# Kernel tuning notes

Measured on AMD Instinct MI355X. Metric: run time of the kernel, lower is better.

The kernel has to match this reference:

```python
import jax, jax.numpy as jnp
import numpy as np

B, CIN, H, W = 16, 32, 256, 256
COUT, KH, KW = 32, 3, 3
NUM_EXPERTS = 8
PAD = ((1, 1), (1, 1))  # static 'same' padding for 3x3, stride 1, dilation 1


def setup_inputs() -> dict:
    key = jax.random.key(0)
    k_x, k_r, k_w, k_b = jax.random.split(key, 4)
    x = jax.random.normal(k_x, (B, CIN, H, W), dtype=jnp.float32)
    # routing weights are typically sigmoid/softmax outputs in [0,1]
    routing_weights = jax.nn.softmax(jax.random.normal(k_r, (B, NUM_EXPERTS), dtype=jnp.float32), axis=-1)
    num_params = COUT * CIN * KH * KW  # groups=1 -> in_channels//groups = CIN
    expert_weight = jax.random.normal(k_w, (NUM_EXPERTS, num_params), dtype=jnp.float32) * 0.05
    expert_bias = jax.random.normal(k_b, (NUM_EXPERTS, COUT), dtype=jnp.float32) * 0.05
    return {"x": x, "routing_weights": routing_weights,
            "expert_weight": expert_weight, "expert_bias": expert_bias}


def reference(x, routing_weights, expert_weight, expert_bias):
    b = x.shape[0]
    # Per-sample kernels: [B, num_params] -> [B, COUT, CIN, KH, KW]
    w = jnp.matmul(routing_weights, expert_weight).reshape(b, COUT, CIN, KH, KW)
    bias = jnp.matmul(routing_weights, expert_bias)  # [B, COUT]

    def conv_one(xi, wi):
        # xi: [CIN, H, W], wi: [COUT, CIN, KH, KW]
        return jax.lax.conv_general_dilated(
            xi[None], wi, window_strides=(1, 1), padding=PAD,
            dimension_numbers=("NCHW", "OIHW", "NCHW"))[0]

    out = jax.vmap(conv_one)(x, w)  # [B, COUT, H, W]
    out = out + bias[:, :, None, None]
    return out
```

## Files before the change

kernel.cpp:

```cpp
#include <hip/hip_runtime.h>

#define B_   16
#define CIN  32
#define COUT 32
#define HH   256
#define WW   256
#define NE   8
#define NTAP 9
#define KTOT (NTAP * CIN)

#define TH 8
#define TW 64
#define LROWS (TH + 2)
#define LCOLS (TW + 2)
#define PXS   40
#define NI    ((TW + 8) / 4)

typedef __attribute__((ext_vector_type(8))) short  short8;
typedef __attribute__((ext_vector_type(4))) float  floatx4;

__device__ __forceinline__ unsigned short f2bf(float f) {
    unsigned int u = __float_as_uint(f);
    u += 0x7FFFu + ((u >> 16) & 1u);
    return (unsigned short)(u >> 16);
}

__global__ __launch_bounds__(256) void prep_weights(
    const float* __restrict__ routing,
    const float* __restrict__ ew,
    const float* __restrict__ eb,
    unsigned short* __restrict__ ws_w,
    float* __restrict__ ws_b)
{
    const int b = blockIdx.x;
    const int t = threadIdx.x;
    float r[NE];
#pragma unroll
    for (int e = 0; e < NE; ++e) r[e] = routing[b * NE + e];

    for (int idx = t; idx < COUT * KTOT; idx += 256) {
        const int co  = idx / KTOT;
        const int k   = idx - co * KTOT;
        const int tap = k >> 5;
        const int ci  = k & 31;
        float acc = 0.f;
#pragma unroll
        for (int e = 0; e < NE; ++e)
            acc += r[e] * ew[e * (COUT * CIN * 9) + co * (CIN * 9) + ci * 9 + tap];
        ws_w[(b * COUT + co) * KTOT + k] = f2bf(acc);
    }
    if (t < COUT) {
        float acc = 0.f;
#pragma unroll
        for (int e = 0; e < NE; ++e) acc += r[e] * eb[e * COUT + t];
        ws_b[b * COUT + t] = acc;
    }
}

__global__ __launch_bounds__(256, 3) void condconv_mfma(
    const float* __restrict__ x,
    const unsigned short* __restrict__ wsw,
    const float* __restrict__ wsb,
    float* __restrict__ out)
{
    __shared__ __align__(16) unsigned short s_x[LROWS * LCOLS * PXS];

    const int b    = blockIdx.z;
    const int x0   = blockIdx.x * TW;
    const int y0   = blockIdx.y * TH;
    const int t    = threadIdx.x;
    const int lane = t & 63;
    const int wv   = t >> 6;
    const int ln   = lane & 15;
    const int quad = lane >> 4;

    for (int task = t; task < LROWS * NI * 4; task += 256) {
        const int cg  = task & 3;
        const int ri  = task >> 2;
        const int i   = ri % NI;
        const int row = ri / NI;
        const int gy  = y0 + row - 1;
        const int gx  = x0 + 4 * i - 4;
        floatx4 v[8];
        if (gy >= 0 && gy < HH && gx >= 0 && gx < WW) {
            const float* src = x + (((size_t)b * CIN + cg * 8) * HH + gy) * WW + gx;
#pragma unroll
            for (int u = 0; u < 8; ++u)
                v[u] = *(const floatx4*)(src + (size_t)u * HH * WW);
        } else {
#pragma unroll
            for (int u = 0; u < 8; ++u) v[u] = (floatx4){0.f, 0.f, 0.f, 0.f};
        }
#pragma unroll
        for (int j = 0; j < 4; ++j) {
            const int lcol = 4 * i + j - 3;
            if (lcol >= 0 && lcol < LCOLS) {
                short8 pk;
#pragma unroll
                for (int u = 0; u < 8; ++u) pk[u] = (short)f2bf(v[u][j]);
                *(short8*)&s_x[(row * LCOLS + lcol) * PXS + cg * 8] = pk;
            }
        }
    }

    const unsigned short* wb = wsw + (size_t)b * COUT * KTOT;
    short8 afc0 = *(const short8*)(wb + ln * KTOT + quad * 8);
    short8 afc1 = *(const short8*)(wb + (16 + ln) * KTOT + quad * 8);

    floatx4 acc[8][2];
#pragma unroll
    for (int tt = 0; tt < 8; ++tt)
#pragma unroll
        for (int h = 0; h < 2; ++h)
            acc[tt][h] = (floatx4){0.f, 0.f, 0.f, 0.f};

    int base[8];
#pragma unroll
    for (int tt = 0; tt < 8; ++tt)
        base[tt] = ((2 * wv + (tt >> 2)) * LCOLS + (tt & 3) * 16 + ln) * PXS + quad * 8;

    __syncthreads();

#pragma unroll 1
    for (int tap = 0; tap < NTAP; ++tap) {
        const int tn = (tap < NTAP - 1) ? tap + 1 : NTAP - 1;
        const short8 afn0 = *(const short8*)(wb + ln * KTOT + tn * 32 + quad * 8);
        const short8 afn1 = *(const short8*)(wb + (16 + ln) * KTOT + tn * 32 + quad * 8);
        const int dy  = tap / 3;
        const int dx  = tap - dy * 3;
        const int off = (dy * LCOLS + dx) * PXS;
#pragma unroll
        for (int tt = 0; tt < 8; ++tt) {
            const short8 bfr = *(const short8*)&s_x[base[tt] + off];
            acc[tt][0] = __builtin_amdgcn_mfma_f32_16x16x32_bf16(afc0, bfr, acc[tt][0], 0, 0, 0);
            acc[tt][1] = __builtin_amdgcn_mfma_f32_16x16x32_bf16(afc1, bfr, acc[tt][1], 0, 0, 0);
        }
        afc0 = afn0;
        afc1 = afn1;
    }

    float bias_v[2][4];
#pragma unroll
    for (int h = 0; h < 2; ++h)
#pragma unroll
        for (int rg = 0; rg < 4; ++rg)
            bias_v[h][rg] = wsb[b * COUT + h * 16 + quad * 4 + rg];

#pragma unroll
    for (int tt = 0; tt < 8; ++tt) {
        const int r  = 2 * wv + (tt >> 2);
        const int q  = tt & 3;
        const int gy = y0 + r;
        const int gx = x0 + q * 16 + ln;
#pragma unroll
        for (int h = 0; h < 2; ++h)
#pragma unroll
            for (int rg = 0; rg < 4; ++rg) {
                const int co = h * 16 + quad * 4 + rg;
                out[(((size_t)b * COUT + co) * HH + gy) * WW + gx] = acc[tt][h][rg] + bias_v[h][rg];
            }
    }
}

extern "C" void kernel_launch(void* const* d_in, const int* in_sizes, int n_in,
                              void* d_out, int out_size, void* d_ws, size_t ws_size,
                              hipStream_t stream) {
    const float* x       = (const float*)d_in[0];
    const float* routing = (const float*)d_in[1];
    const float* ew      = (const float*)d_in[2];
    const float* eb      = (const float*)d_in[3];
    float* out = (float*)d_out;

    unsigned short* ws_w = (unsigned short*)d_ws;
    float* ws_b = (float*)((char*)d_ws + (size_t)B_ * COUT * KTOT * 2);

    prep_weights<<<dim3(B_), dim3(256), 0, stream>>>(routing, ew, eb, ws_w, ws_b);

    dim3 grid(WW / TW, HH / TH, B_);
    condconv_mfma<<<grid, dim3(256), 0, stream>>>(x, ws_w, ws_b, out);
}
```

Before: 287.2 us.

## Swap MFMA operands for vectorized stores and halve tile width

Swaps the MFMA A/B operands so pixels are the row dimension and output channels the column dimension. Each lane then holds four consecutive x positions for one output channel and writes them as a single 16-byte store instead of scattered scalar stores. The tile width is halved to 32 and the occupancy hint raised to 5 blocks per CU, which gives more, smaller blocks. The cost is more halo overhead per block, since the input tile is still loaded with a 2-column halo on each side for only 32 columns.

```diff
diff --git a/kernel.cpp b/kernel.cpp
--- a/kernel.cpp
+++ b/kernel.cpp
@@ -10,7 +10,7 @@
 #define KTOT (NTAP * CIN)
 
 #define TH 8
-#define TW 64
+#define TW 32
 #define LROWS (TH + 2)
 #define LCOLS (TW + 2)
 #define PXS   40
@@ -57,7 +57,7 @@
     }
 }
 
-__global__ __launch_bounds__(256, 3) void condconv_mfma(
+__global__ __launch_bounds__(256, 5) void condconv_mfma(
     const float* __restrict__ x,
     const unsigned short* __restrict__ wsw,
     const float* __restrict__ wsb,
@@ -104,61 +104,57 @@
     }
 
     const unsigned short* wb = wsw + (size_t)b * COUT * KTOT;
-    short8 afc0 = *(const short8*)(wb + ln * KTOT + quad * 8);
-    short8 afc1 = *(const short8*)(wb + (16 + ln) * KTOT + quad * 8);
+    short8 wfc0 = *(const short8*)(wb + ln * KTOT + quad * 8);
+    short8 wfc1 = *(const short8*)(wb + (16 + ln) * KTOT + quad * 8);
 
-    floatx4 acc[8][2];
+    floatx4 acc[4][2];
 #pragma unroll
-    for (int tt = 0; tt < 8; ++tt)
+    for (int tt = 0; tt < 4; ++tt)
 #pragma unroll
         for (int h = 0; h < 2; ++h)
             acc[tt][h] = (floatx4){0.f, 0.f, 0.f, 0.f};
 
-    int base[8];
+    int base[4];
 #pragma unroll
-    for (int tt = 0; tt < 8; ++tt)
-        base[tt] = ((2 * wv + (tt >> 2)) * LCOLS + (tt & 3) * 16 + ln) * PXS + quad * 8;
+    for (int tt = 0; tt < 4; ++tt)
+        base[tt] = ((2 * wv + (tt >> 1)) * LCOLS + (tt & 1) * 16 + ln) * PXS + quad * 8;
 
     __syncthreads();
 
 #pragma unroll 1
     for (int tap = 0; tap < NTAP; ++tap) {
         const int tn = (tap < NTAP - 1) ? tap + 1 : NTAP - 1;
-        const short8 afn0 = *(const short8*)(wb + ln * KTOT + tn * 32 + quad * 8);
-        const short8 afn1 = *(const short8*)(wb + (16 + ln) * KTOT + tn * 32 + quad * 8);
+        const short8 wfn0 = *(const short8*)(wb + ln * KTOT + tn * 32 + quad * 8);
+        const short8 wfn1 = *(const short8*)(wb + (16 + ln) * KTOT + tn * 32 + quad * 8);
         const int dy  = tap / 3;
         const int dx  = tap - dy * 3;
         const int off = (dy * LCOLS + dx) * PXS;
 #pragma unroll
-        for (int tt = 0; tt < 8; ++tt) {
-            const short8 bfr = *(const short8*)&s_x[base[tt] + off];
-            acc[tt][0] = __builtin_amdgcn_mfma_f32_16x16x32_bf16(afc0, bfr, acc[tt][0], 0, 0, 0);
-            acc[tt][1] = __builtin_amdgcn_mfma_f32_16x16x32_bf16(afc1, bfr, acc[tt][1], 0, 0, 0);
+        for (int tt = 0; tt < 4; ++tt) {
+            const short8 pfr = *(const short8*)&s_x[base[tt] + off];
+            acc[tt][0] = __builtin_amdgcn_mfma_f32_16x16x32_bf16(pfr, wfc0, acc[tt][0], 0, 0, 0);
+            acc[tt][1] = __builtin_amdgcn_mfma_f32_16x16x32_bf16(pfr, wfc1, acc[tt][1], 0, 0, 0);
         }
-        afc0 = afn0;
-        afc1 = afn1;
+        wfc0 = wfn0;
+        wfc1 = wfn1;
     }
 
-    float bias_v[2][4];
-#pragma unroll
-    for (int h = 0; h < 2; ++h)
-#pragma unroll
-        for (int rg = 0; rg < 4; ++rg)
-            bias_v[h][rg] = wsb[b * COUT + h * 16 + quad * 4 + rg];
+    float bias_v[2];
+    bias_v[0] = wsb[b * COUT + ln];
+    bias_v[1] = wsb[b * COUT + 16 + ln];
 
 #pragma unroll
-    for (int tt = 0; tt < 8; ++tt) {
-        const int r  = 2 * wv + (tt >> 2);
-        const int q  = tt & 3;
-        const int gy = y0 + r;
-        const int gx = x0 + q * 16 + ln;
+    for (int tt = 0; tt < 4; ++tt) {
+        const int gy = y0 + 2 * wv + (tt >> 1);
+        const int gx = x0 + (tt & 1) * 16 + quad * 4;
 #pragma unroll
-        for (int h = 0; h < 2; ++h)
+        for (int h = 0; h < 2; ++h) {
+            floatx4 vo = acc[tt][h];
 #pragma unroll
-            for (int rg = 0; rg < 4; ++rg) {
-                const int co = h * 16 + quad * 4 + rg;
-                out[(((size_t)b * COUT + co) * HH + gy) * WW + gx] = acc[tt][h][rg] + bias_v[h][rg];
-            }
+            for (int e = 0; e < 4; ++e) vo[e] += bias_v[h];
+            const int co = h * 16 + ln;
+            *(floatx4*)(out + (((size_t)b * COUT + co) * HH + gy) * WW + gx) = vo;
+        }
     }
 }
 
```

New measurement: 289.0 us. About the same (+0.6%).
